# Kernel optimization log

Measured on AMD Instinct MI355X. Metric: run time of the kernel, lower is better.

Reference implementation:

```python
import jax, jax.numpy as jnp
import numpy as np
from jax import lax

BN_EPS = 1e-5


def setup_inputs() -> dict:
    key = jax.random.key(0)
    ks = jax.random.split(key, 8)
    B, C, H, W = 2, 256, 64, 64
    Cr = C // 4
    return {
        "x": jax.random.normal(ks[0], (B, C, H, W), jnp.float32),
        "conv_w": jax.random.normal(ks[1], (Cr, C, 3, 3), jnp.float32) * 0.02,
        "conv_b": jax.random.normal(ks[2], (Cr,), jnp.float32) * 0.02,
        "bn_gamma": jax.random.uniform(ks[3], (Cr,), jnp.float32, 0.5, 1.5),
        "bn_beta": jax.random.normal(ks[4], (Cr,), jnp.float32) * 0.1,
        "bn_mean": jax.random.normal(ks[5], (Cr,), jnp.float32) * 0.1,
        "bn_var": jax.random.uniform(ks[6], (Cr,), jnp.float32, 0.5, 1.5),
        "prelu_w": jnp.full((1,), 0.25, jnp.float32),
    }


def reference(x, conv_w, conv_b, bn_gamma, bn_beta, bn_mean, bn_var, prelu_w):
    B, C, H, W = x.shape
    N = H * W
    # conv_match: 3x3 conv (pad=1) -> BatchNorm (inference) -> PReLU
    y = lax.conv_general_dilated(
        x, conv_w, window_strides=(1, 1), padding="SAME",
        dimension_numbers=("NCHW", "OIHW", "NCHW"))
    y = y + conv_b[None, :, None, None]
    scale = bn_gamma / jnp.sqrt(bn_var + BN_EPS)
    y = (y - bn_mean[None, :, None, None]) * scale[None, :, None, None] + bn_beta[None, :, None, None]
    y = jnp.where(y >= 0, y, prelu_w[0] * y)  # PReLU, single shared slope

    e = y.reshape(B, -1, N)                       # [B, Cr, N]
    sim = jnp.einsum("bdn,bdm->bnm", e, e)        # [B, N, N]
    sim = sim - jnp.max(sim, axis=2, keepdims=True)

    # sparsemax along last dim
    srt = -jnp.sort(-sim, axis=2)                 # descending sort
    cs = jnp.cumsum(srt, axis=2) - 1.0
    ar = jnp.arange(1, N + 1, dtype=sim.dtype)[None, None, :]
    mask = ar * srt > cs
    k = jnp.sum(mask, axis=2, keepdims=True)      # int support size, [B,N,1]
    tau = jnp.take_along_axis(cs, k - 1, axis=2) / k.astype(sim.dtype)
    p = jnp.maximum(sim - tau, 0.0)               # sparsemax probs [B,N,N]

    out = jnp.einsum("bcn,bnm->bcm", x.reshape(B, C, N), p)
    return out.reshape(B, C, H, W) + x
```

## Files before the change

### kernel.cpp

```cpp
#include <hip/hip_runtime.h>
#include <math.h>

#define NPIX 4096
#define CR   64
#define CIN  256
#define HW   64
#define RB   8
#define CSPLIT 8

typedef __attribute__((ext_vector_type(8))) short s16x8;
typedef __attribute__((ext_vector_type(4))) float f32x4;

__device__ __forceinline__ unsigned short f2bf(float f) {
  union { float f; unsigned u; } a; a.f = f;
  return (unsigned short)((a.u + 0x7FFF + ((a.u >> 16) & 1)) >> 16);
}

__global__ __launch_bounds__(256) void k_conv_part(
    const float* __restrict__ x, const float* __restrict__ cw,
    float* __restrict__ pp) {
  const int hg = blockIdx.x;
  const int dg = blockIdx.y;
  const int b  = blockIdx.z >> 3;
  const int cs = blockIdx.z & 7;
  const int h0 = hg * 2, d0 = dg * 32, c0 = cs * 32;
  const int tid = threadIdx.x;
  const int wp = tid & 31;
  const int dq = tid >> 5;
  const int w0 = wp * 2;

  __shared__ float xs[16][4][68];
  __shared__ float wl[16][9][32];

  float acc[2][2][4] = {};

  for (int cc = 0; cc < 32; cc += 16) {
    __syncthreads();
    for (int i = tid; i < 16 * 256; i += 256) {
      int c = i >> 8, r = (i >> 6) & 3, w = i & 63;
      int row = h0 - 1 + r;
      float v = 0.f;
      if (row >= 0 && row < HW)
        v = x[((size_t)(b * CIN + c0 + cc + c) << 12) + row * HW + w];
      xs[c][r][w + 1] = v;
    }
    if (tid < 128) {
      int c = tid >> 3, r = (tid >> 1) & 3, s = tid & 1;
      xs[c][r][s ? 65 : 0] = 0.f;
    }
    for (int i = tid; i < 16 * 9 * 32; i += 256) {
      int c = i / 288, rem = i - c * 288, tap = rem >> 5, d = rem & 31;
      wl[c][tap][d] = cw[(size_t)(d0 + d) * 2304 + (c0 + cc + c) * 9 + tap];
    }
    __syncthreads();

#pragma unroll 2
    for (int c = 0; c < 16; ++c) {
      float xv[4][4];
#pragma unroll
      for (int r = 0; r < 4; ++r) {
        float2 p0 = *(const float2*)&xs[c][r][w0];
        float2 p1 = *(const float2*)&xs[c][r][w0 + 2];
        xv[r][0] = p0.x; xv[r][1] = p0.y; xv[r][2] = p1.x; xv[r][3] = p1.y;
      }
#pragma unroll
      for (int tap = 0; tap < 9; ++tap) {
        const int kh = tap / 3, kw = tap - kh * 3;
        float4 wv = *(const float4*)&wl[c][tap][dq * 4];
        float wf[4] = {wv.x, wv.y, wv.z, wv.w};
#pragma unroll
        for (int hi = 0; hi < 2; ++hi)
#pragma unroll
          for (int wi = 0; wi < 2; ++wi) {
            float xvv = xv[hi + kh][wi + kw];
#pragma unroll
            for (int di = 0; di < 4; ++di)
              acc[hi][wi][di] = fmaf(wf[di], xvv, acc[hi][wi][di]);
          }
      }
    }
  }
#pragma unroll
  for (int di = 0; di < 4; ++di) {
    int d = d0 + dq * 4 + di;
#pragma unroll
    for (int hi = 0; hi < 2; ++hi)
#pragma unroll
      for (int wi = 0; wi < 2; ++wi)
        pp[((size_t)((b * CSPLIT + cs) * 64 + d) << 12) + (h0 + hi) * HW + w0 + wi] =
            acc[hi][wi][di];
  }
}

__global__ __launch_bounds__(256) void k_bn(
    const float* __restrict__ pp, const float* __restrict__ cb,
    const float* __restrict__ gamma, const float* __restrict__ beta,
    const float* __restrict__ mean, const float* __restrict__ var,
    const float* __restrict__ pw, float* __restrict__ e) {
  const int flat = blockIdx.x * 256 + threadIdx.x;
  const int b = flat >> 18;
  const int d = (flat >> 12) & 63;
  const int n = flat & 4095;
  float s = 0.f;
#pragma unroll
  for (int cs = 0; cs < CSPLIT; ++cs)
    s += pp[((size_t)((b * CSPLIT + cs) * 64 + d) << 12) + n];
  float scale = gamma[d] / sqrtf(var[d] + 1e-5f);
  float y = (s + cb[d] - mean[d]) * scale + beta[d];
  y = (y >= 0.f) ? y : pw[0] * y;
  e[((size_t)(b * CR + d) << 12) + n] = y;
}

__global__ __launch_bounds__(512) void k_gsm(
    const float* __restrict__ e, unsigned short* __restrict__ p,
    unsigned char* __restrict__ flags) {
  const int n0 = blockIdx.x * RB;
  const int b  = blockIdx.y;
  const int tid = threadIdx.x;
  const int lane = tid & 63, wid = tid >> 6;
  const float* eb = e + ((size_t)b * CR << 12);

  __shared__ float er[CR][RB];
  __shared__ float ssum[8][RB];
  __shared__ int   scnt[8][RB];
  __shared__ float stau[RB];
  __shared__ int   sprev[RB];
  __shared__ int   schg;

  {
    int d = tid >> 3, r = tid & 7;
    er[d][r] = eb[((size_t)d << 12) + n0 + r];
  }
  if (tid < RB) sprev[tid] = NPIX;
  __syncthreads();

  float acc[RB][8];
#pragma unroll
  for (int r = 0; r < RB; ++r)
#pragma unroll
    for (int j = 0; j < 8; ++j) acc[r][j] = 0.f;

  const int m0 = tid * 8;
  for (int d = 0; d < CR; ++d) {
    const float4* row = (const float4*)(eb + ((size_t)d << 12) + m0);
    float4 c0 = row[0], c1 = row[1];
    float cv[8] = {c0.x, c0.y, c0.z, c0.w, c1.x, c1.y, c1.z, c1.w};
    float4 r0 = *(const float4*)&er[d][0];
    float4 r1 = *(const float4*)&er[d][4];
    float rv[RB] = {r0.x, r0.y, r0.z, r0.w, r1.x, r1.y, r1.z, r1.w};
#pragma unroll
    for (int r = 0; r < RB; ++r)
#pragma unroll
      for (int j = 0; j < 8; ++j)
        acc[r][j] = fmaf(rv[r], cv[j], acc[r][j]);
  }

  float lm[RB];
#pragma unroll
  for (int r = 0; r < RB; ++r) {
    float m = acc[r][0];
#pragma unroll
    for (int j = 1; j < 8; ++j) m = fmaxf(m, acc[r][j]);
    lm[r] = m;
  }
#pragma unroll
  for (int o = 32; o > 0; o >>= 1)
#pragma unroll
    for (int r = 0; r < RB; ++r) lm[r] = fmaxf(lm[r], __shfl_down(lm[r], o));
  if (lane == 0)
#pragma unroll
    for (int r = 0; r < RB; ++r) ssum[wid][r] = lm[r];
  __syncthreads();
  if (tid < RB) {
    float m = ssum[0][tid];
#pragma unroll
    for (int w = 1; w < 8; ++w) m = fmaxf(m, ssum[w][tid]);
    stau[tid] = m - 1.0f;
  }

  float ls[RB];
  int lc[RB];
  for (int it = 0; it < 100; ++it) {
    __syncthreads();
    float tl[RB];
#pragma unroll
    for (int r = 0; r < RB; ++r) tl[r] = stau[r];
    if (tid == 0) schg = 0;
#pragma unroll
    for (int r = 0; r < RB; ++r) {
      float t = 0.f; int c = 0;
#pragma unroll
      for (int j = 0; j < 8; ++j)
        if (acc[r][j] > tl[r]) { t += acc[r][j]; ++c; }
      ls[r] = t; lc[r] = c;
    }
#pragma unroll
    for (int o = 32; o > 0; o >>= 1)
#pragma unroll
      for (int r = 0; r < RB; ++r) {
        ls[r] += __shfl_down(ls[r], o);
        lc[r] += __shfl_down(lc[r], o);
      }
    if (lane == 0)
#pragma unroll
      for (int r = 0; r < RB; ++r) { ssum[wid][r] = ls[r]; scnt[wid][r] = lc[r]; }
    __syncthreads();
    if (tid < RB) {
      float s = 0.f; int c = 0;
#pragma unroll
      for (int w = 0; w < 8; ++w) { s += ssum[w][tid]; c += scnt[w][tid]; }
      stau[tid] = (s - 1.f) / (float)c;
      if (c != sprev[tid]) { sprev[tid] = c; schg = 1; }
    }
    __syncthreads();
    if (schg == 0) break;
  }

  unsigned short* pr = p + (((size_t)b << 12) + n0) * (size_t)NPIX + m0;
  int any = 0;
#pragma unroll
  for (int r = 0; r < RB; ++r) {
    float tr = stau[r];
    s16x8 o0;
#pragma unroll
    for (int j = 0; j < 8; ++j) {
      float pv = fmaxf(acc[r][j] - tr, 0.f);
      any |= (pv > 0.f);
      o0[j] = (short)f2bf(pv);
    }
    *(s16x8*)(pr + (size_t)r * NPIX) = o0;
  }
  if (any)
    flags[((size_t)b << 12) | ((size_t)(tid >> 4) << 7) | (size_t)(n0 >> 5)] = 1;
}

__global__ __launch_bounds__(256) void k_out_mfma(
    const unsigned short* __restrict__ pb, const float* __restrict__ x,
    float* __restrict__ out, const unsigned char* __restrict__ flags) {
  const int m0 = blockIdx.x * 128;
  const int c0 = blockIdx.y * 64;
  const int b  = blockIdx.z;
  const int tid = threadIdx.x;
  const int l = tid & 63, wid = tid >> 6;
  const int wr = wid >> 1, wc = wid & 1;

  __shared__ unsigned short As[64][42];
  __shared__ unsigned short Bs[128][42];
  __shared__ unsigned char fl[128];

  if (tid < 128)
    fl[tid] = flags[((size_t)b << 12) | ((size_t)blockIdx.x << 7) | (size_t)tid];

  f32x4 acc[2][4];
#pragma unroll
  for (int i = 0; i < 2; ++i)
#pragma unroll
    for (int j = 0; j < 4; ++j)
#pragma unroll
      for (int q = 0; q < 4; ++q) acc[i][j][q] = 0.f;

  const int arow = tid >> 2;
  const int akc  = (tid & 3) * 8;
  const float* axsrc = x + ((size_t)(b * CIN + c0 + arow) << 12) + akc;
  const int bm = (tid & 31) * 4;
  const int bk = (tid >> 5) * 4;
  const unsigned short* bsrc = pb + ((size_t)(b * NPIX + bk) << 12) + m0 + bm;

  __syncthreads();

  for (int k0 = 0; k0 < NPIX; k0 += 32) {
    if (!fl[k0 >> 5]) continue;
    __syncthreads();
    float4 A0 = *(const float4*)(axsrc + k0);
    float4 A1 = *(const float4*)(axsrc + k0 + 4);
    s16x8 ap;
    ap[0] = (short)f2bf(A0.x); ap[1] = (short)f2bf(A0.y);
    ap[2] = (short)f2bf(A0.z); ap[3] = (short)f2bf(A0.w);
    ap[4] = (short)f2bf(A1.x); ap[5] = (short)f2bf(A1.y);
    ap[6] = (short)f2bf(A1.z); ap[7] = (short)f2bf(A1.w);
    *(s16x8*)&As[arow][akc] = ap;
    const unsigned short* bp = bsrc + ((size_t)k0 << 12);
    ushort4 L0 = *(const ushort4*)(bp);
    ushort4 L1 = *(const ushort4*)(bp + 4096);
    ushort4 L2 = *(const ushort4*)(bp + 8192);
    ushort4 L3 = *(const ushort4*)(bp + 12288);
    *(ushort4*)&Bs[bm + 0][bk] = make_ushort4(L0.x, L1.x, L2.x, L3.x);
    *(ushort4*)&Bs[bm + 1][bk] = make_ushort4(L0.y, L1.y, L2.y, L3.y);
    *(ushort4*)&Bs[bm + 2][bk] = make_ushort4(L0.z, L1.z, L2.z, L3.z);
    *(ushort4*)&Bs[bm + 3][bk] = make_ushort4(L0.w, L1.w, L2.w, L3.w);
    __syncthreads();

    s16x8 a[2], bb[4];
    const int kg = l >> 4;
#pragma unroll
    for (int i = 0; i < 2; ++i) {
      int row = wr * 32 + i * 16 + (l & 15);
      a[i] = *(const s16x8*)&As[row][kg * 8];
    }
#pragma unroll
    for (int j = 0; j < 4; ++j) {
      int n = wc * 64 + j * 16 + (l & 15);
      bb[j] = *(const s16x8*)&Bs[n][kg * 8];
    }
#pragma unroll
    for (int i = 0; i < 2; ++i)
#pragma unroll
      for (int j = 0; j < 4; ++j)
        acc[i][j] = __builtin_amdgcn_mfma_f32_16x16x32_bf16(
            a[i], bb[j], acc[i][j], 0, 0, 0);
  }

#pragma unroll
  for (int i = 0; i < 2; ++i)
#pragma unroll
    for (int j = 0; j < 4; ++j)
#pragma unroll
      for (int q = 0; q < 4; ++q) {
        int c = c0 + wr * 32 + i * 16 + (l >> 4) * 4 + q;
        int m = m0 + wc * 64 + j * 16 + (l & 15);
        size_t off = ((size_t)(b * CIN + c) << 12) + m;
        out[off] = acc[i][j][q] + x[off];
      }
}

extern "C" void kernel_launch(void* const* d_in, const int* in_sizes, int n_in,
                              void* d_out, int out_size, void* d_ws, size_t ws_size,
                              hipStream_t stream) {
  const float* x     = (const float*)d_in[0];
  const float* cw    = (const float*)d_in[1];
  const float* cb    = (const float*)d_in[2];
  const float* gamma = (const float*)d_in[3];
  const float* beta  = (const float*)d_in[4];
  const float* mean  = (const float*)d_in[5];
  const float* var   = (const float*)d_in[6];
  const float* pw    = (const float*)d_in[7];
  float* out = (float*)d_out;

  unsigned short* p_bf = (unsigned short*)d_ws;
  float* pp   = (float*)((char*)d_ws + ((size_t)64 << 20));
  float* e    = (float*)((char*)d_ws + ((size_t)80 << 20));
  unsigned char* flags = (unsigned char*)((char*)d_ws + ((size_t)84 << 20));

  hipMemsetAsync(flags, 0, 2 * 32 * 128, stream);
  k_conv_part<<<dim3(32, 2, 16), 256, 0, stream>>>(x, cw, pp);
  k_bn<<<2048, 256, 0, stream>>>(pp, cb, gamma, beta, mean, var, pw, e);
  k_gsm<<<dim3(NPIX / RB, 2), 512, 0, stream>>>(e, p_bf, flags);
  k_out_mfma<<<dim3(32, 4, 2), 256, 0, stream>>>(p_bf, x, out, flags);
}
```

Measured before the change: 273.0 us.

## Compute similarity matrix with split-bf16 MFMA and transposed embedding layout

```diff
diff --git a/kernel.cpp b/kernel.cpp
--- a/kernel.cpp
+++ b/kernel.cpp
@@ -5,7 +5,6 @@
 #define CR   64
 #define CIN  256
 #define HW   64
-#define RB   8
 #define CSPLIT 8
 
 typedef __attribute__((ext_vector_type(8))) short s16x8;
@@ -14,6 +13,9 @@
 __device__ __forceinline__ unsigned short f2bf(float f) {
   union { float f; unsigned u; } a; a.f = f;
   return (unsigned short)((a.u + 0x7FFF + ((a.u >> 16) & 1)) >> 16);
+}
+__device__ __forceinline__ float bf2f(unsigned short h) {
+  union { unsigned u; float f; } a; a.u = (unsigned)h << 16; return a.f;
 }
 
 __global__ __launch_bounds__(256) void k_conv_part(
@@ -96,142 +98,174 @@
     const float* __restrict__ pp, const float* __restrict__ cb,
     const float* __restrict__ gamma, const float* __restrict__ beta,
     const float* __restrict__ mean, const float* __restrict__ var,
-    const float* __restrict__ pw, float* __restrict__ e) {
-  const int flat = blockIdx.x * 256 + threadIdx.x;
-  const int b = flat >> 18;
-  const int d = (flat >> 12) & 63;
-  const int n = flat & 4095;
-  float s = 0.f;
-#pragma unroll
-  for (int cs = 0; cs < CSPLIT; ++cs)
-    s += pp[((size_t)((b * CSPLIT + cs) * 64 + d) << 12) + n];
-  float scale = gamma[d] / sqrtf(var[d] + 1e-5f);
-  float y = (s + cb[d] - mean[d]) * scale + beta[d];
-  y = (y >= 0.f) ? y : pw[0] * y;
-  e[((size_t)(b * CR + d) << 12) + n] = y;
-}
-
-__global__ __launch_bounds__(512) void k_gsm(
-    const float* __restrict__ e, unsigned short* __restrict__ p,
-    unsigned char* __restrict__ flags) {
-  const int n0 = blockIdx.x * RB;
+    const float* __restrict__ pw, unsigned short* __restrict__ eTh,
+    unsigned short* __restrict__ eTl) {
+  const int n0 = blockIdx.x * 64;
   const int b  = blockIdx.y;
   const int tid = threadIdx.x;
-  const int lane = tid & 63, wid = tid >> 6;
-  const float* eb = e + ((size_t)b * CR << 12);
-
-  __shared__ float er[CR][RB];
-  __shared__ float ssum[8][RB];
-  __shared__ int   scnt[8][RB];
-  __shared__ float stau[RB];
-  __shared__ int   sprev[RB];
+  __shared__ float et[64][65];
+
+  const float slope = pw[0];
+#pragma unroll 4
+  for (int dd = 0; dd < 16; ++dd) {
+    int d = dd * 4 + (tid >> 6);
+    int n = tid & 63;
+    float s = 0.f;
+#pragma unroll
+    for (int cs = 0; cs < CSPLIT; ++cs)
+      s += pp[((size_t)((b * CSPLIT + cs) * 64 + d) << 12) + n0 + n];
+    float scale = gamma[d] / sqrtf(var[d] + 1e-5f);
+    float y = (s + cb[d] - mean[d]) * scale + beta[d];
+    y = (y >= 0.f) ? y : slope * y;
+    et[d][n] = y;
+  }
+  __syncthreads();
+#pragma unroll 4
+  for (int w = 0; w < 16; ++w) {
+    int n = w * 4 + (tid >> 6);
+    int d = tid & 63;
+    float v = et[d][n];
+    unsigned short hi = f2bf(v);
+    unsigned short lo = f2bf(v - bf2f(hi));
+    size_t off = (((size_t)b << 12) + n0 + n) * 64 + d;
+    eTh[off] = hi;
+    eTl[off] = lo;
+  }
+}
+
+__global__ __launch_bounds__(1024) void k_gsm(
+    const unsigned short* __restrict__ eTh, const unsigned short* __restrict__ eTl,
+    unsigned short* __restrict__ p, unsigned char* __restrict__ flags) {
+  const int n0 = blockIdx.x * 16;
+  const int b  = blockIdx.y;
+  const int tid = threadIdx.x;
+  const int l = tid & 63, wid = tid >> 6;
+  const int lc = l & 15, lq = l >> 4;
+
+  __shared__ __align__(16) unsigned short eah[16][72];
+  __shared__ __align__(16) unsigned short eal[16][72];
+  __shared__ float rs[16][16];
+  __shared__ int   rc[16][16];
+  __shared__ float stau[16];
+  __shared__ int   sprev[16];
   __shared__ int   schg;
 
+  const size_t ebase = ((size_t)b << 12) * 64;
+
   {
-    int d = tid >> 3, r = tid & 7;
-    er[d][r] = eb[((size_t)d << 12) + n0 + r];
-  }
-  if (tid < RB) sprev[tid] = NPIX;
+    int d = tid & 63, r = (tid >> 6) & 15;
+    size_t off = ebase + (size_t)(n0 + r) * 64 + d;
+    eah[r][d] = eTh[off];
+    eal[r][d] = eTl[off];
+  }
+  if (tid < 16) sprev[tid] = NPIX + 1;
   __syncthreads();
 
-  float acc[RB][8];
-#pragma unroll
-  for (int r = 0; r < RB; ++r)
-#pragma unroll
-    for (int j = 0; j < 8; ++j) acc[r][j] = 0.f;
-
-  const int m0 = tid * 8;
-  for (int d = 0; d < CR; ++d) {
-    const float4* row = (const float4*)(eb + ((size_t)d << 12) + m0);
-    float4 c0 = row[0], c1 = row[1];
-    float cv[8] = {c0.x, c0.y, c0.z, c0.w, c1.x, c1.y, c1.z, c1.w};
-    float4 r0 = *(const float4*)&er[d][0];
-    float4 r1 = *(const float4*)&er[d][4];
-    float rv[RB] = {r0.x, r0.y, r0.z, r0.w, r1.x, r1.y, r1.z, r1.w};
-#pragma unroll
-    for (int r = 0; r < RB; ++r)
-#pragma unroll
-      for (int j = 0; j < 8; ++j)
-        acc[r][j] = fmaf(rv[r], cv[j], acc[r][j]);
-  }
-
-  float lm[RB];
-#pragma unroll
-  for (int r = 0; r < RB; ++r) {
-    float m = acc[r][0];
-#pragma unroll
-    for (int j = 1; j < 8; ++j) m = fmaxf(m, acc[r][j]);
-    lm[r] = m;
-  }
-#pragma unroll
-  for (int o = 32; o > 0; o >>= 1)
-#pragma unroll
-    for (int r = 0; r < RB; ++r) lm[r] = fmaxf(lm[r], __shfl_down(lm[r], o));
-  if (lane == 0)
-#pragma unroll
-    for (int r = 0; r < RB; ++r) ssum[wid][r] = lm[r];
+  f32x4 acc[16];
+#pragma unroll
+  for (int t = 0; t < 16; ++t)
+#pragma unroll
+    for (int q = 0; q < 4; ++q) acc[t][q] = 0.f;
+
+  const int mbase = wid * 256;
+#pragma unroll
+  for (int kc = 0; kc < 2; ++kc) {
+    s16x8 ah = *(const s16x8*)&eah[lc][kc * 32 + lq * 8];
+    s16x8 al = *(const s16x8*)&eal[lc][kc * 32 + lq * 8];
+#pragma unroll
+    for (int t = 0; t < 16; ++t) {
+      size_t off = ebase + (size_t)(mbase + t * 16 + lc) * 64 + kc * 32 + lq * 8;
+      s16x8 bh = *(const s16x8*)&eTh[off];
+      s16x8 bl = *(const s16x8*)&eTl[off];
+      acc[t] = __builtin_amdgcn_mfma_f32_16x16x32_bf16(ah, bh, acc[t], 0, 0, 0);
+      acc[t] = __builtin_amdgcn_mfma_f32_16x16x32_bf16(ah, bl, acc[t], 0, 0, 0);
+      acc[t] = __builtin_amdgcn_mfma_f32_16x16x32_bf16(al, bh, acc[t], 0, 0, 0);
+    }
+  }
+
+  {
+    float mx[4];
+#pragma unroll
+    for (int q = 0; q < 4; ++q) {
+      float m = acc[0][q];
+#pragma unroll
+      for (int t = 1; t < 16; ++t) m = fmaxf(m, acc[t][q]);
+      mx[q] = m;
+    }
+#pragma unroll
+    for (int o = 1; o <= 8; o <<= 1)
+#pragma unroll
+      for (int q = 0; q < 4; ++q) mx[q] = fmaxf(mx[q], __shfl_xor(mx[q], o));
+    if (lc == 0)
+#pragma unroll
+      for (int q = 0; q < 4; ++q) rs[wid][lq * 4 + q] = mx[q];
+  }
   __syncthreads();
-  if (tid < RB) {
-    float m = ssum[0][tid];
-#pragma unroll
-    for (int w = 1; w < 8; ++w) m = fmaxf(m, ssum[w][tid]);
+  if (tid < 16) {
+    float m = rs[0][tid];
+#pragma unroll
+    for (int w = 1; w < 16; ++w) m = fmaxf(m, rs[w][tid]);
     stau[tid] = m - 1.0f;
   }
 
-  float ls[RB];
-  int lc[RB];
-  for (int it = 0; it < 100; ++it) {
-    __syncthreads();
-    float tl[RB];
-#pragma unroll
-    for (int r = 0; r < RB; ++r) tl[r] = stau[r];
+  for (int it = 0; it < 64; ++it) {
+    __syncthreads();
+    float tl[4];
+#pragma unroll
+    for (int q = 0; q < 4; ++q) tl[q] = stau[lq * 4 + q];
     if (tid == 0) schg = 0;
-#pragma unroll
-    for (int r = 0; r < RB; ++r) {
-      float t = 0.f; int c = 0;
-#pragma unroll
-      for (int j = 0; j < 8; ++j)
-        if (acc[r][j] > tl[r]) { t += acc[r][j]; ++c; }
-      ls[r] = t; lc[r] = c;
-    }
-#pragma unroll
-    for (int o = 32; o > 0; o >>= 1)
-#pragma unroll
-      for (int r = 0; r < RB; ++r) {
-        ls[r] += __shfl_down(ls[r], o);
-        lc[r] += __shfl_down(lc[r], o);
-      }
-    if (lane == 0)
-#pragma unroll
-      for (int r = 0; r < RB; ++r) { ssum[wid][r] = ls[r]; scnt[wid][r] = lc[r]; }
-    __syncthreads();
-    if (tid < RB) {
-      float s = 0.f; int c = 0;
-#pragma unroll
-      for (int w = 0; w < 8; ++w) { s += ssum[w][tid]; c += scnt[w][tid]; }
-      stau[tid] = (s - 1.f) / (float)c;
-      if (c != sprev[tid]) { sprev[tid] = c; schg = 1; }
+    float s[4]; int c[4];
+#pragma unroll
+    for (int q = 0; q < 4; ++q) { s[q] = 0.f; c[q] = 0; }
+#pragma unroll
+    for (int t = 0; t < 16; ++t)
+#pragma unroll
+      for (int q = 0; q < 4; ++q) {
+        float v = acc[t][q];
+        if (v > tl[q]) { s[q] += v; ++c[q]; }
+      }
+#pragma unroll
+    for (int o = 1; o <= 8; o <<= 1)
+#pragma unroll
+      for (int q = 0; q < 4; ++q) {
+        s[q] += __shfl_xor(s[q], o);
+        c[q] += __shfl_xor(c[q], o);
+      }
+    if (lc == 0)
+#pragma unroll
+      for (int q = 0; q < 4; ++q) { rs[wid][lq * 4 + q] = s[q]; rc[wid][lq * 4 + q] = c[q]; }
+    __syncthreads();
+    if (tid < 16) {
+      float ss = 0.f; int cc = 0;
+#pragma unroll
+      for (int w = 0; w < 16; ++w) { ss += rs[w][tid]; cc += rc[w][tid]; }
+      stau[tid] = (ss - 1.f) / (float)cc;
+      if (cc != sprev[tid]) { sprev[tid] = cc; schg = 1; }
     }
     __syncthreads();
     if (schg == 0) break;
   }
 
-  unsigned short* pr = p + (((size_t)b << 12) + n0) * (size_t)NPIX + m0;
-  int any = 0;
-#pragma unroll
-  for (int r = 0; r < RB; ++r) {
-    float tr = stau[r];
-    s16x8 o0;
-#pragma unroll
-    for (int j = 0; j < 8; ++j) {
-      float pv = fmaxf(acc[r][j] - tr, 0.f);
-      any |= (pv > 0.f);
-      o0[j] = (short)f2bf(pv);
-    }
-    *(s16x8*)(pr + (size_t)r * NPIX) = o0;
-  }
-  if (any)
-    flags[((size_t)b << 12) | ((size_t)(tid >> 4) << 7) | (size_t)(n0 >> 5)] = 1;
+  float tw[4];
+#pragma unroll
+  for (int q = 0; q < 4; ++q) tw[q] = stau[lq * 4 + q];
+  int any0 = 0, any1 = 0;
+#pragma unroll
+  for (int t = 0; t < 16; ++t) {
+#pragma unroll
+    for (int q = 0; q < 4; ++q) {
+      float pv = fmaxf(acc[t][q] - tw[q], 0.f);
+      if (t < 8) any0 |= (pv > 0.f); else any1 |= (pv > 0.f);
+      p[((size_t)(b * NPIX + n0 + lq * 4 + q) << 12) + mbase + t * 16 + lc] =
+          f2bf(pv);
+    }
+  }
+  unsigned long long b0 = __ballot(any0), b1 = __ballot(any1);
+  if (l == 0) {
+    int kt = n0 >> 5;
+    if (b0) flags[(b << 12) | ((wid * 2 + 0) << 7) | kt] = 1;
+    if (b1) flags[(b << 12) | ((wid * 2 + 1) << 7) | kt] = 1;
+  }
 }
 
 __global__ __launch_bounds__(256) void k_out_mfma(
@@ -337,13 +371,15 @@
   float* out = (float*)d_out;
 
   unsigned short* p_bf = (unsigned short*)d_ws;
-  float* pp   = (float*)((char*)d_ws + ((size_t)64 << 20));
-  float* e    = (float*)((char*)d_ws + ((size_t)80 << 20));
+  float* pp  = (float*)((char*)d_ws + ((size_t)64 << 20));
+  unsigned short* eTh = (unsigned short*)((char*)d_ws + ((size_t)80 << 20));
+  unsigned short* eTl = (unsigned short*)((char*)d_ws + ((size_t)81 << 20));
   unsigned char* flags = (unsigned char*)((char*)d_ws + ((size_t)84 << 20));
 
   hipMemsetAsync(flags, 0, 2 * 32 * 128, stream);
   k_conv_part<<<dim3(32, 2, 16), 256, 0, stream>>>(x, cw, pp);
-  k_bn<<<2048, 256, 0, stream>>>(pp, cb, gamma, beta, mean, var, pw, e);
-  k_gsm<<<dim3(NPIX / RB, 2), 512, 0, stream>>>(e, p_bf, flags);
+  k_bn<<<dim3(64, 2), 256, 0, stream>>>(pp, cb, gamma, beta, mean, var, pw,
+                                        eTh, eTl);
+  k_gsm<<<dim3(NPIX / 16, 2), 1024, 0, stream>>>(eTh, eTl, p_bf, flags);
   k_out_mfma<<<dim3(32, 4, 2), 256, 0, stream>>>(p_bf, x, out, flags);
 }
```

Result: slower. 295.0 us (+8.1%).
